# Kernel optimization log

Measured on AMD Instinct MI355X. Metric: run time of the kernel, lower is better.

## Reference

```python
import jax, jax.numpy as jnp
import numpy as np

B, C, T, H = 64, 800, 512, 1024
IN = 2 * C  # 1600, matches hardcoded input_size in PCLSTMCell


def setup_inputs() -> dict:
    key = jax.random.key(0)
    ks = jax.random.split(key, 24)
    s = 0.02
    d = {}
    d["x"] = jax.random.normal(ks[0], (B, C, T), jnp.float32)
    d["y"] = jax.random.normal(ks[1], (B, C, T), jnp.float32)
    d["subject_id"] = jax.random.normal(ks[2], (B, 87), jnp.float32)
    for n_i, n in enumerate(["f", "i", "u", "o"]):
        d[f"W_{n}x"] = jax.random.normal(ks[3 + 4 * n_i], (IN, H), jnp.float32) * s
        d[f"b_{n}x"] = jnp.zeros((H,), jnp.float32)
        d[f"W_{n}h"] = jax.random.normal(ks[4 + 4 * n_i], (H, H), jnp.float32) * s
        d[f"b_{n}h"] = jnp.zeros((H,), jnp.float32)
    d["W_init"] = jax.random.normal(ks[20], (87, H), jnp.float32) * s
    d["b_init"] = jnp.zeros((H,), jnp.float32)
    return d


def reference(x, y, subject_id,
              W_fx, b_fx, W_fh, b_fh,
              W_ix, b_ix, W_ih, b_ih,
              W_ux, b_ux, W_uh, b_uh,
              W_ox, b_ox, W_oh, b_oh,
              W_init, b_init):
    Bc, Cc, Tc = x.shape
    Hc = W_fh.shape[0]
    # y_prev[t] = y[t-1], zeros at t=0 (matches torch.zeros at t==0)
    y_prev = jnp.concatenate([jnp.zeros_like(y[..., :1]), y[..., :-1]], axis=-1)
    # torch.stack((x_i, y_prev), dim=-1).view(B,-1): channel-interleaved [x0,y0,x1,y1,...]
    xs = jnp.stack([x, y_prev], axis=2)                    # [B, C, 2, T]
    xs = jnp.moveaxis(xs, -1, 0).reshape(Tc, Bc, 2 * Cc)    # [T, B, 2C]
    # fuse the 4 input-side gate GEMMs and precompute over all timesteps
    Wx = jnp.concatenate([W_fx, W_ix, W_ux, W_ox], axis=1)  # [2C, 4H]
    bx = jnp.concatenate([b_fx, b_ix, b_ux, b_ox])          # [4H]
    gx = jnp.einsum('tbi,ig->tbg', xs, Wx) + bx             # [T, B, 4H]
    Wh = jnp.concatenate([W_fh, W_ih, W_uh, W_oh], axis=1)  # [H, 4H]
    bh = jnp.concatenate([b_fh, b_ih, b_uh, b_oh])

    h0 = jnp.zeros((Bc, Hc), x.dtype)
    c0 = subject_id @ W_init + b_init                       # initilaizer(subject_id)

    def step(carry, gx_t):
        h, c = carry
        g = gx_t + h @ Wh + bh
        f, i, u, o = jnp.split(g, 4, axis=-1)
        f = jax.nn.sigmoid(f)
        i = jax.nn.sigmoid(i)
        u = jnp.tanh(u)
        o = jax.nn.sigmoid(o)
        c = c * f + i * u
        h = o * jnp.tanh(c)
        return (h, c), h

    (_, c_fin), hs = jax.lax.scan(step, (h0, c0), gx)       # hs: [T, B, H]
    h_seq = jnp.moveaxis(hs, 0, -1)                          # [B, H, T]
    return h_seq, c_fin
```

## Files before the change

kernel.cpp:

```cpp
#include <hip/hip_runtime.h>

typedef __attribute__((ext_vector_type(8))) short short8;
typedef __attribute__((ext_vector_type(4))) float f32x4;
typedef __attribute__((ext_vector_type(4))) _Float16 f16x4;
typedef unsigned long long u64_t;

#define DI __device__ __forceinline__

DI unsigned short f2bf(float f) {
  unsigned int u = __float_as_uint(f);
  u += 0x7FFFu + ((u >> 16) & 1u);
  return (unsigned short)(u >> 16);
}

DI void gload_lds16(const void* g, void* l) {
  __builtin_amdgcn_global_load_lds(
      (const __attribute__((address_space(1))) unsigned int*)g,
      (__attribute__((address_space(3))) unsigned int*)l, 16, 0, 0);
}

DI float sigm(float x) { return 1.f / (1.f + __expf(-x)); }
DI float tanh_(float x) { return 1.f - 2.f / (__expf(2.f * x) + 1.f); }

static constexpr size_t OFF_WXT  = 0;
static constexpr size_t OFF_WHT  = 13107200;
static constexpr size_t OFF_BSUM = OFF_WHT + 8388608;
static constexpr size_t OFF_XS   = OFF_BSUM + 16384;
static constexpr size_t OFF_GX   = OFF_XS + 104857600;
static constexpr size_t OFF_HBUF = OFF_GX + 268435456;
static constexpr size_t OFF_BAR  = OFF_HBUF + 262144;
static constexpr size_t WS_NEED  = OFF_BAR + 2048;

__global__ __launch_bounds__(256) void pack_w(
    const float* __restrict__ s0, const float* __restrict__ s1,
    const float* __restrict__ s2, const float* __restrict__ s3,
    unsigned short* __restrict__ dst, int K) {
  __shared__ float tile[32][33];
  const int tx = threadIdx.x & 31, ty = threadIdx.x >> 5;
  const int kt = blockIdx.x, nt = blockIdx.y;
  const int q = (nt * 32) >> 10;
  const float* src = (q == 0) ? s0 : (q == 1) ? s1 : (q == 2) ? s2 : s3;
  const int cbase = (nt * 32) & 1023;
#pragma unroll
  for (int i = 0; i < 4; ++i) {
    int k = kt * 32 + ty + i * 8;
    tile[ty + i * 8][tx] = src[(size_t)k * 1024 + cbase + tx];
  }
  __syncthreads();
#pragma unroll
  for (int i = 0; i < 4; ++i) {
    int n = nt * 32 + ty + i * 8;
    dst[(size_t)n * K + kt * 32 + tx] = f2bf(tile[tx][ty + i * 8]);
  }
}

__global__ __launch_bounds__(256) void pack_bias(
    const float* bx0, const float* bx1, const float* bx2, const float* bx3,
    const float* bh0, const float* bh1, const float* bh2, const float* bh3,
    float* __restrict__ bsum) {
  int n = blockIdx.x * 256 + threadIdx.x;
  int q = n >> 10, j = n & 1023;
  const float* bx = (q == 0) ? bx0 : (q == 1) ? bx1 : (q == 2) ? bx2 : bx3;
  const float* bh = (q == 0) ? bh0 : (q == 1) ? bh1 : (q == 2) ? bh2 : bh3;
  bsum[n] = bx[j] + bh[j];
}

__global__ __launch_bounds__(256) void xs_pack(
    const float* __restrict__ x, const float* __restrict__ y,
    unsigned int* __restrict__ xs32) {
  __shared__ float xt[32][33], yt[32][33];
  const int tx = threadIdx.x & 31, ty = threadIdx.x >> 5;
  const int tt = blockIdx.x, ct = blockIdx.y, b = blockIdx.z;
#pragma unroll
  for (int i = 0; i < 4; ++i) {
    int c = ct * 32 + ty + i * 8;
    int t = tt * 32 + tx;
    size_t base = ((size_t)b * 800 + c) * 512;
    xt[ty + i * 8][tx] = x[base + t];
    yt[ty + i * 8][tx] = (t == 0) ? 0.f : y[base + t - 1];
  }
  __syncthreads();
#pragma unroll
  for (int i = 0; i < 4; ++i) {
    int t = tt * 32 + ty + i * 8;
    int c = ct * 32 + tx;
    unsigned int pk = ((unsigned int)f2bf(yt[tx][ty + i * 8]) << 16) |
                      (unsigned int)f2bf(xt[tx][ty + i * 8]);
    xs32[((size_t)t * 64 + b) * 800 + c] = pk;
  }
}

__global__ __launch_bounds__(256, 2) void gemm_gx(
    const unsigned short* __restrict__ xs, const unsigned short* __restrict__ Wxt,
    const float* __restrict__ bsum, _Float16* __restrict__ gx) {
  __shared__ __align__(16) unsigned short Al[128 * 64];
  __shared__ __align__(16) unsigned short Bl[128 * 64];
  const int tid = threadIdx.x;
  const int w = tid >> 6, l = tid & 63;
  const int l15 = l & 15, l4 = l >> 4;
  const int wm = w >> 1, wn = w & 1;
  const int u = (blockIdx.x & 7) * 1024 + (blockIdx.x >> 3);
  const int bm = u >> 5, bn = u & 31;

  f32x4 acc[4][4];
#pragma unroll
  for (int i = 0; i < 4; ++i)
#pragma unroll
    for (int j = 0; j < 4; ++j) acc[i][j] = (f32x4){0.f, 0.f, 0.f, 0.f};

  const int srow = w * 8 + (l >> 3);
  const int scol = (l & 7) * 8;

  for (int kt = 0; kt < 25; ++kt) {
#pragma unroll
    for (int rnd = 0; rnd < 4; ++rnd) {
      int row = rnd * 32 + srow;
      gload_lds16(xs + ((size_t)(bm * 128 + row)) * 1600 + kt * 64 + scol,
                  Al + rnd * 2048 + w * 512);
      gload_lds16(Wxt + ((size_t)(bn * 128 + row)) * 1600 + kt * 64 + scol,
                  Bl + rnd * 2048 + w * 512);
    }
    __syncthreads();
#pragma unroll
    for (int kk = 0; kk < 64; kk += 32) {
      short8 av[4], bv[4];
#pragma unroll
      for (int mf = 0; mf < 4; ++mf)
        av[mf] = *(const short8*)&Al[(wm * 64 + mf * 16 + l15) * 64 + kk + l4 * 8];
#pragma unroll
      for (int nf = 0; nf < 4; ++nf)
        bv[nf] = *(const short8*)&Bl[(wn * 64 + nf * 16 + l15) * 64 + kk + l4 * 8];
#pragma unroll
      for (int mf = 0; mf < 4; ++mf)
#pragma unroll
        for (int nf = 0; nf < 4; ++nf)
          acc[mf][nf] = __builtin_amdgcn_mfma_f32_16x16x32_bf16(
              av[mf], bv[nf], acc[mf][nf], 0, 0, 0);
    }
    __syncthreads();
  }
#pragma unroll
  for (int nf = 0; nf < 4; ++nf) {
    int col = bn * 128 + wn * 64 + nf * 16 + l15;
    float bs = bsum[col];
    int colp = (col & 1023) * 4 + (col >> 10);
#pragma unroll
    for (int mf = 0; mf < 4; ++mf) {
      int row0 = bm * 128 + wm * 64 + mf * 16 + l4 * 4;
#pragma unroll
      for (int j = 0; j < 4; ++j)
        gx[(size_t)(row0 + j) * 4096 + colp] = (_Float16)(acc[mf][nf][j] + bs);
    }
  }
}

__global__ __launch_bounds__(512, 2) void lstm_seq(
    const _Float16* __restrict__ gx, const unsigned short* __restrict__ Wht,
    const float* __restrict__ subj, const float* __restrict__ Winit,
    const float* __restrict__ binit, float* __restrict__ out,
    unsigned int* __restrict__ hbuf, unsigned int* __restrict__ bar) {
  const int gg  = blockIdx.x & 7;
  const int cwg = blockIdx.x >> 3;
  const int tid = threadIdx.x;
  const int w = tid >> 6, l = tid & 63;
  const int l15 = l & 15, l4 = l >> 4;
  const int ws = w & 1, kq = w >> 1;
  const int ghc = cwg * 32 + ws * 16 + l15;

  __shared__ __align__(16) char smem[98304];
  char* part = smem + 16384;

  short8 Bf[32];
  {
    const unsigned short* wp =
        Wht + (size_t)(cwg * 32 + ws * 16 + l15) * 1024 + kq * 256 + l4 * 8;
#pragma unroll
    for (int g = 0; g < 4; ++g)
#pragma unroll
      for (int ks = 0; ks < 8; ++ks)
        Bf[g * 8 + ks] = *(const short8*)(wp + (size_t)g * 1048576 + ks * 32);
  }

  float c[4], hq[4][8];
  if (w < 2 && l4 < 2) {
#pragma unroll
    for (int j = 0; j < 4; ++j) {
      int b = gg * 8 + l4 * 4 + j;
      float a = binit[ghc];
      for (int k = 0; k < 87; ++k) a += subj[b * 87 + k] * Winit[k * 1024 + ghc];
      c[j] = a;
    }
  }

  unsigned int* flags = bar + gg * 32;
  const u64_t* hb64 = (const u64_t*)hbuf;

  for (int t8 = 0; t8 < 64; ++t8) {
#pragma unroll
    for (int s = 0; s < 8; ++s) {
      const int t = t8 * 8 + s;
      const int cur = s & 1, nxt = cur ^ 1;
      if (w == 7) {
        const unsigned tgt = (unsigned)t;
        for (;;) {
          unsigned f = 0xFFFFFFFFu;
          if (l < 32)
            f = __hip_atomic_load(flags + l, __ATOMIC_RELAXED, __HIP_MEMORY_SCOPE_AGENT);
          if (__all(f >= tgt)) break;
          __builtin_amdgcn_s_sleep(2);
        }
      }
      __syncthreads();
      {
        const u64_t* src = hb64 + (gg * 2 + cur) * 2048;
#pragma unroll
        for (int i = 0; i < 4; ++i) {
          int idx = i * 512 + tid;
          int row = idx >> 8, pp = idx & 255;
          u64_t v = __hip_atomic_load((u64_t*)(src + row * 256 + pp),
                                      __ATOMIC_RELAXED, __HIP_MEMORY_SCOPE_AGENT);
          *(u64_t*)(smem + ((row * 2048 + pp * 8) ^ ((row & 7) << 4))) = v;
        }
      }
      f16x4 gxq[4];
      if (w < 2 && l4 < 2) {
        const _Float16* gp =
            gx + ((size_t)(t * 64 + gg * 8 + l4 * 4)) * 4096 + ghc * 4;
#pragma unroll
        for (int j = 0; j < 4; ++j) gxq[j] = *(const f16x4*)(gp + (size_t)j * 4096);
      }
      __syncthreads();
      f32x4 acc[4];
#pragma unroll
      for (int g = 0; g < 4; ++g) acc[g] = (f32x4){0.f, 0.f, 0.f, 0.f};
#pragma unroll
      for (int ks = 0; ks < 8; ++ks) {
        short8 a = *(const short8*)(
            smem + (((l15 & 7) * 2048 + kq * 512 + ks * 64 + l4 * 16) ^ ((l15 & 7) << 4)));
#pragma unroll
        for (int g = 0; g < 4; ++g)
          acc[g] = __builtin_amdgcn_mfma_f32_16x16x32_bf16(a, Bf[g * 8 + ks], acc[g], 0, 0, 0);
      }
      if (w >= 2) {
        char* pb = part + (ws * 3 + kq - 1) * 4096;
#pragma unroll
        for (int g = 0; g < 4; ++g) *(f32x4*)(pb + g * 1024 + l * 16) = acc[g];
      }
      __syncthreads();
      if (w < 2) {
        f32x4 red[4];
#pragma unroll
        for (int g = 0; g < 4; ++g) {
          red[g] = acc[g];
#pragma unroll
          for (int kk = 0; kk < 3; ++kk)
            red[g] += *(const f32x4*)(part + (ws * 3 + kk) * 4096 + g * 1024 + l * 16);
        }
        if (l4 < 2) {
#pragma unroll
          for (int j = 0; j < 4; ++j) {
            float fv = sigm(red[0][j] + (float)gxq[j][0]);
            float iv = sigm(red[1][j] + (float)gxq[j][1]);
            float uv = tanh_(red[2][j] + (float)gxq[j][2]);
            float ov = sigm(red[3][j] + (float)gxq[j][3]);
            c[j] = c[j] * fv + iv * uv;
            float hv = ov * tanh_(c[j]);
            hq[j][s] = hv;
            float hn = __shfl_xor(hv, 1);
            if (!(l15 & 1)) {
              unsigned int pk = (unsigned int)f2bf(hv) | ((unsigned int)f2bf(hn) << 16);
              __hip_atomic_store(
                  hbuf + (gg * 2 + nxt) * 4096 + (l4 * 4 + j) * 512 +
                      cwg * 16 + ws * 8 + (l15 >> 1),
                  pk, __ATOMIC_RELAXED, __HIP_MEMORY_SCOPE_AGENT);
            }
          }
        }
      }
      asm volatile("s_waitcnt vmcnt(0)" ::: "memory");
      __syncthreads();
      if (tid == 0)
        __hip_atomic_store(bar + gg * 32 + cwg, (unsigned)(t + 1),
                           __ATOMIC_RELAXED, __HIP_MEMORY_SCOPE_AGENT);
    }
    if (w < 2 && l4 < 2) {
      int tb = t8 * 8;
#pragma unroll
      for (int j = 0; j < 4; ++j) {
        f32x4 v0 = {hq[j][0], hq[j][1], hq[j][2], hq[j][3]};
        f32x4 v1 = {hq[j][4], hq[j][5], hq[j][6], hq[j][7]};
        float* op = out + (size_t)(gg * 8 + l4 * 4 + j) * 524288 + (size_t)ghc * 512 + tb;
        *(f32x4*)op = v0;
        *(f32x4*)(op + 4) = v1;
      }
    }
  }
  if (w < 2 && l4 < 2) {
#pragma unroll
    for (int j = 0; j < 4; ++j)
      out[33554432 + (size_t)(gg * 8 + l4 * 4 + j) * 1024 + ghc] = c[j];
  }
}

extern "C" void kernel_launch(void* const* d_in, const int* in_sizes, int n_in,
                              void* d_out, int out_size, void* d_ws, size_t ws_size,
                              hipStream_t stream) {
  (void)in_sizes; (void)n_in; (void)out_size;
  if (ws_size < WS_NEED) return;

  const float* x     = (const float*)d_in[0];
  const float* y     = (const float*)d_in[1];
  const float* subj  = (const float*)d_in[2];
  const float* W_fx  = (const float*)d_in[3];
  const float* b_fx  = (const float*)d_in[4];
  const float* W_fh  = (const float*)d_in[5];
  const float* b_fh  = (const float*)d_in[6];
  const float* W_ix  = (const float*)d_in[7];
  const float* b_ix  = (const float*)d_in[8];
  const float* W_ih  = (const float*)d_in[9];
  const float* b_ih  = (const float*)d_in[10];
  const float* W_ux  = (const float*)d_in[11];
  const float* b_ux  = (const float*)d_in[12];
  const float* W_uh  = (const float*)d_in[13];
  const float* b_uh  = (const float*)d_in[14];
  const float* W_ox  = (const float*)d_in[15];
  const float* b_ox  = (const float*)d_in[16];
  const float* W_oh  = (const float*)d_in[17];
  const float* b_oh  = (const float*)d_in[18];
  const float* Winit = (const float*)d_in[19];
  const float* binit = (const float*)d_in[20];
  float* out = (float*)d_out;

  char* ws = (char*)d_ws;
  unsigned short* Wxt  = (unsigned short*)(ws + OFF_WXT);
  unsigned short* Wht  = (unsigned short*)(ws + OFF_WHT);
  float*          bsum = (float*)(ws + OFF_BSUM);
  unsigned int*   xs32 = (unsigned int*)(ws + OFF_XS);
  _Float16*       gx   = (_Float16*)(ws + OFF_GX);
  unsigned int*   hbuf = (unsigned int*)(ws + OFF_HBUF);
  unsigned int*   bar  = (unsigned int*)(ws + OFF_BAR);

  hipMemsetAsync(ws + OFF_HBUF, 0, WS_NEED - OFF_HBUF, stream);

  pack_w<<<dim3(50, 128), 256, 0, stream>>>(W_fx, W_ix, W_ux, W_ox, Wxt, 1600);
  pack_w<<<dim3(32, 128), 256, 0, stream>>>(W_fh, W_ih, W_uh, W_oh, Wht, 1024);
  pack_bias<<<16, 256, 0, stream>>>(b_fx, b_ix, b_ux, b_ox, b_fh, b_ih, b_uh, b_oh, bsum);
  xs_pack<<<dim3(16, 25, 64), 256, 0, stream>>>(x, y, xs32);
  gemm_gx<<<8192, 256, 0, stream>>>((const unsigned short*)xs32, Wxt, bsum, gx);

  const _Float16* gxc = gx;
  const unsigned short* whtc = Wht;
  void* ka[8] = {(void*)&gxc, (void*)&whtc, (void*)&subj, (void*)&Winit,
                 (void*)&binit, (void*)&out, (void*)&hbuf, (void*)&bar};
  hipError_t e = hipLaunchCooperativeKernel((const void*)lstm_seq, dim3(256), dim3(512),
                                            ka, 0, stream);
  if (e != hipSuccess) {
    lstm_seq<<<256, 512, 0, stream>>>(gxc, whtc, subj, Winit, binit, out, hbuf, bar);
  }
}
```

Baseline: 3.217 ms.

## Read h directly from L2 per wave and use per-wave flags instead of block barriers

Each wave now polls the per-wave step flags itself and loads its A fragments of the previous hidden state straight from global memory with cache-bypassing (sc0 sc1) loads. This removes the LDS staging copy and the two __syncthreads around it. Partial-sum buffers are double-buffered in LDS by step parity. Each reducing wave publishes its own flag after its h stores drain, and the next step's gx values are prefetched early. The aim is to shorten the per-timestep critical path of this latency-bound recurrence, at the cost of more redundant global traffic, busy spinning without sleep, and subtler memory-ordering assumptions.

Measured after the change: 5.804 ms. 80.4% more time.

```diff
diff --git a/kernel.cpp b/kernel.cpp
--- a/kernel.cpp
+++ b/kernel.cpp
@@ -21,6 +21,19 @@
 
 DI float sigm(float x) { return 1.f / (1.f + __expf(-x)); }
 DI float tanh_(float x) { return 1.f - 2.f / (__expf(2.f * x) + 1.f); }
+
+template <int OFF>
+DI short8 llc_load16(const char* p) {
+  short8 r;
+  asm volatile("global_load_dwordx4 %0, %1, off offset:%2 sc0 sc1"
+               : "=v"(r) : "v"(p), "i"(OFF) : "memory");
+  return r;
+}
+DI u64_t cached_load8(const char* p) {
+  u64_t r;
+  asm volatile("global_load_dwordx2 %0, %1, off" : "=v"(r) : "v"(p) : "memory");
+  return r;
+}
 
 static constexpr size_t OFF_WXT  = 0;
 static constexpr size_t OFF_WHT  = 13107200;
@@ -29,7 +42,7 @@
 static constexpr size_t OFF_GX   = OFF_XS + 104857600;
 static constexpr size_t OFF_HBUF = OFF_GX + 268435456;
 static constexpr size_t OFF_BAR  = OFF_HBUF + 262144;
-static constexpr size_t WS_NEED  = OFF_BAR + 2048;
+static constexpr size_t WS_NEED  = OFF_BAR + 4096;
 
 __global__ __launch_bounds__(256) void pack_w(
     const float* __restrict__ s0, const float* __restrict__ s1,
@@ -168,7 +181,6 @@
   const int ghc = cwg * 32 + ws * 16 + l15;
 
   __shared__ __align__(16) char smem[98304];
-  char* part = smem + 16384;
 
   short8 Bf[32];
   {
@@ -181,7 +193,7 @@
         Bf[g * 8 + ks] = *(const short8*)(wp + (size_t)g * 1048576 + ks * 32);
   }
 
-  float c[4], hq[4][8];
+  float c[4], hq[4][4];
   if (w < 2 && l4 < 2) {
 #pragma unroll
     for (int j = 0; j < 4; ++j) {
@@ -192,57 +204,51 @@
     }
   }
 
-  unsigned int* flags = bar + gg * 32;
-  const u64_t* hb64 = (const u64_t*)hbuf;
-
-  for (int t8 = 0; t8 < 64; ++t8) {
-#pragma unroll
-    for (int s = 0; s < 8; ++s) {
-      const int t = t8 * 8 + s;
-      const int cur = s & 1, nxt = cur ^ 1;
-      if (w == 7) {
+  unsigned int* flags = bar + gg * 64;
+  u64_t gxp[4];
+  if (w < 2 && l4 < 2) {
+    const char* gp = (const char*)(gx + ((size_t)(gg * 8 + l4 * 4)) * 4096 + ghc * 4);
+#pragma unroll
+    for (int j = 0; j < 4; ++j) gxp[j] = cached_load8(gp + (size_t)j * 8192);
+  }
+
+  for (int t4 = 0; t4 < 128; ++t4) {
+#pragma unroll
+    for (int s = 0; s < 4; ++s) {
+      const int t = t4 * 4 + s;
+      const int cur = t & 1;
+      {
         const unsigned tgt = (unsigned)t;
         for (;;) {
-          unsigned f = 0xFFFFFFFFu;
-          if (l < 32)
-            f = __hip_atomic_load(flags + l, __ATOMIC_RELAXED, __HIP_MEMORY_SCOPE_AGENT);
+          unsigned f = __hip_atomic_load(flags + l, __ATOMIC_RELAXED,
+                                         __HIP_MEMORY_SCOPE_AGENT);
           if (__all(f >= tgt)) break;
-          __builtin_amdgcn_s_sleep(2);
         }
       }
-      __syncthreads();
-      {
-        const u64_t* src = hb64 + (gg * 2 + cur) * 2048;
-#pragma unroll
-        for (int i = 0; i < 4; ++i) {
-          int idx = i * 512 + tid;
-          int row = idx >> 8, pp = idx & 255;
-          u64_t v = __hip_atomic_load((u64_t*)(src + row * 256 + pp),
-                                      __ATOMIC_RELAXED, __HIP_MEMORY_SCOPE_AGENT);
-          *(u64_t*)(smem + ((row * 2048 + pp * 8) ^ ((row & 7) << 4))) = v;
-        }
-      }
-      f16x4 gxq[4];
-      if (w < 2 && l4 < 2) {
-        const _Float16* gp =
-            gx + ((size_t)(t * 64 + gg * 8 + l4 * 4)) * 4096 + ghc * 4;
-#pragma unroll
-        for (int j = 0; j < 4; ++j) gxq[j] = *(const f16x4*)(gp + (size_t)j * 4096);
-      }
-      __syncthreads();
+      const char* ab = (const char*)hbuf + (size_t)(gg * 2 + cur) * 16384 +
+                       (l15 & 7) * 2048 + kq * 512 + l4 * 16;
+      short8 av[8];
+      av[0] = llc_load16<0>(ab);
+      av[1] = llc_load16<64>(ab);
+      av[2] = llc_load16<128>(ab);
+      av[3] = llc_load16<192>(ab);
+      av[4] = llc_load16<256>(ab);
+      av[5] = llc_load16<320>(ab);
+      av[6] = llc_load16<384>(ab);
+      av[7] = llc_load16<448>(ab);
+      asm volatile("s_waitcnt vmcnt(0)" ::: "memory");
+      __builtin_amdgcn_sched_barrier(0);
       f32x4 acc[4];
 #pragma unroll
       for (int g = 0; g < 4; ++g) acc[g] = (f32x4){0.f, 0.f, 0.f, 0.f};
 #pragma unroll
-      for (int ks = 0; ks < 8; ++ks) {
-        short8 a = *(const short8*)(
-            smem + (((l15 & 7) * 2048 + kq * 512 + ks * 64 + l4 * 16) ^ ((l15 & 7) << 4)));
+      for (int ks = 0; ks < 8; ++ks)
 #pragma unroll
         for (int g = 0; g < 4; ++g)
-          acc[g] = __builtin_amdgcn_mfma_f32_16x16x32_bf16(a, Bf[g * 8 + ks], acc[g], 0, 0, 0);
-      }
+          acc[g] = __builtin_amdgcn_mfma_f32_16x16x32_bf16(av[ks], Bf[g * 8 + ks],
+                                                           acc[g], 0, 0, 0);
       if (w >= 2) {
-        char* pb = part + (ws * 3 + kq - 1) * 4096;
+        char* pb = smem + (size_t)((cur * 6) + (ws * 3 + kq - 1)) * 4096;
 #pragma unroll
         for (int g = 0; g < 4; ++g) *(f32x4*)(pb + g * 1024 + l * 16) = acc[g];
       }
@@ -254,15 +260,17 @@
           red[g] = acc[g];
 #pragma unroll
           for (int kk = 0; kk < 3; ++kk)
-            red[g] += *(const f32x4*)(part + (ws * 3 + kk) * 4096 + g * 1024 + l * 16);
+            red[g] += *(const f32x4*)(smem + (size_t)((cur * 6) + (ws * 3 + kk)) * 4096 +
+                                      g * 1024 + l * 16);
         }
         if (l4 < 2) {
 #pragma unroll
           for (int j = 0; j < 4; ++j) {
-            float fv = sigm(red[0][j] + (float)gxq[j][0]);
-            float iv = sigm(red[1][j] + (float)gxq[j][1]);
-            float uv = tanh_(red[2][j] + (float)gxq[j][2]);
-            float ov = sigm(red[3][j] + (float)gxq[j][3]);
+            union { u64_t q; f16x4 v; } gu; gu.q = gxp[j];
+            float fv = sigm(red[0][j] + (float)gu.v[0]);
+            float iv = sigm(red[1][j] + (float)gu.v[1]);
+            float uv = tanh_(red[2][j] + (float)gu.v[2]);
+            float ov = sigm(red[3][j] + (float)gu.v[3]);
             c[j] = c[j] * fv + iv * uv;
             float hv = ov * tanh_(c[j]);
             hq[j][s] = hv;
@@ -270,28 +278,31 @@
             if (!(l15 & 1)) {
               unsigned int pk = (unsigned int)f2bf(hv) | ((unsigned int)f2bf(hn) << 16);
               __hip_atomic_store(
-                  hbuf + (gg * 2 + nxt) * 4096 + (l4 * 4 + j) * 512 +
+                  hbuf + (size_t)(gg * 2 + (cur ^ 1)) * 4096 + (l4 * 4 + j) * 512 +
                       cwg * 16 + ws * 8 + (l15 >> 1),
                   pk, __ATOMIC_RELAXED, __HIP_MEMORY_SCOPE_AGENT);
             }
           }
         }
+        asm volatile("s_waitcnt vmcnt(0)" ::: "memory");
+        if (l == 0)
+          __hip_atomic_store(flags + cwg * 2 + ws, (unsigned)(t + 1),
+                             __ATOMIC_RELAXED, __HIP_MEMORY_SCOPE_AGENT);
+        if (l4 < 2) {
+          int tn = (t < 511) ? t + 1 : t;
+          const char* gp =
+              (const char*)(gx + ((size_t)(tn * 64 + gg * 8 + l4 * 4)) * 4096 + ghc * 4);
+#pragma unroll
+          for (int j = 0; j < 4; ++j) gxp[j] = cached_load8(gp + (size_t)j * 8192);
+        }
       }
-      asm volatile("s_waitcnt vmcnt(0)" ::: "memory");
-      __syncthreads();
-      if (tid == 0)
-        __hip_atomic_store(bar + gg * 32 + cwg, (unsigned)(t + 1),
-                           __ATOMIC_RELAXED, __HIP_MEMORY_SCOPE_AGENT);
     }
     if (w < 2 && l4 < 2) {
-      int tb = t8 * 8;
+      int tb = t4 * 4;
 #pragma unroll
       for (int j = 0; j < 4; ++j) {
-        f32x4 v0 = {hq[j][0], hq[j][1], hq[j][2], hq[j][3]};
-        f32x4 v1 = {hq[j][4], hq[j][5], hq[j][6], hq[j][7]};
-        float* op = out + (size_t)(gg * 8 + l4 * 4 + j) * 524288 + (size_t)ghc * 512 + tb;
-        *(f32x4*)op = v0;
-        *(f32x4*)(op + 4) = v1;
+        f32x4 v = {hq[j][0], hq[j][1], hq[j][2], hq[j][3]};
+        *(f32x4*)(out + (size_t)(gg * 8 + l4 * 4 + j) * 524288 + (size_t)ghc * 512 + tb) = v;
       }
     }
   }
```
